# Performance work log

Hardware: AMD Instinct MI355X
Metric: run time of the kernel (lower is better)

The kernel has to match this reference:

```python
import jax, jax.numpy as jnp
import numpy as np

N_NODES = 100000
N_GRAPHS = 512


def gcn_conv(x, W, b, src, dst, n):
    # PyG GCNConv: h = x @ W; add self-loops; sym-normalize; scatter-add to dst; + bias
    h = x @ W
    loop = jnp.arange(n, dtype=src.dtype)
    s = jnp.concatenate([src, loop])
    d = jnp.concatenate([dst, loop])
    deg = jax.ops.segment_sum(jnp.ones_like(d, dtype=h.dtype), d, num_segments=n)
    dinv = jnp.where(deg > 0, jax.lax.rsqrt(deg), 0.0)
    norm = dinv[s] * dinv[d]               # [E+N]
    msg = h[s] * norm[:, None]             # gather + scale
    out = jax.ops.segment_sum(msg, d, num_segments=n)
    return out + b


def setup_inputs() -> dict:
    key = jax.random.key(0)
    ks = jax.random.split(key, 12)
    F_in, H, C = 128, 128, 10
    x = jax.random.normal(ks[0], (N_NODES, F_in), dtype=jnp.float32)
    edge_index = jax.random.randint(ks[1], (2, 3200000), 0, N_NODES, dtype=jnp.int64)
    batch = jnp.sort(jax.random.randint(ks[2], (N_NODES,), 0, N_GRAPHS, dtype=jnp.int64))
    def glorot(k, fi, fo):
        s = jnp.sqrt(6.0 / (fi + fo))
        return jax.random.uniform(k, (fi, fo), dtype=jnp.float32, minval=-s, maxval=s)
    return {
        "x": x, "edge_index": edge_index, "batch": batch,
        "W_in": glorot(ks[3], F_in, H), "b_in": jnp.zeros((H,), jnp.float32),
        "W_h0": glorot(ks[4], H, H), "b_h0": jnp.zeros((H,), jnp.float32),
        "W_h1": glorot(ks[5], H, H), "b_h1": jnp.zeros((H,), jnp.float32),
        "W_out": glorot(ks[6], H, C), "b_out": jnp.zeros((C,), jnp.float32),
    }


def reference(x, edge_index, batch, W_in, b_in, W_h0, b_h0, W_h1, b_h1, W_out, b_out):
    src, dst = edge_index[0], edge_index[1]
    n = x.shape[0]
    h = jax.nn.relu(gcn_conv(x, W_in, b_in, src, dst, n))
    h = jax.nn.relu(gcn_conv(h, W_h0, b_h0, src, dst, n))
    h = jax.nn.relu(gcn_conv(h, W_h1, b_h1, src, dst, n))
    h = gcn_conv(h, W_out, b_out, src, dst, n)
    # global_mean_pool over graph ids
    sums = jax.ops.segment_sum(h, batch, num_segments=N_GRAPHS)
    cnts = jax.ops.segment_sum(jnp.ones((n,), h.dtype), batch, num_segments=N_GRAPHS)
    pooled = sums / jnp.maximum(cnts, 1.0)[:, None]
    return jax.nn.log_softmax(pooled, axis=-1)
```

## Files before the change

kernel.cpp:

```cpp
#include <hip/hip_runtime.h>
#include <math.h>

#define TPB 256
#define MAXDEG 80
#define SHIFT 8
#define BNODES 256
#define CAP 10240
#define EPB 4096
#define LSTR 136
#define NCHUNK 13

typedef short bf16x8 __attribute__((ext_vector_type(8)));
typedef float f32x4 __attribute__((ext_vector_type(4)));

__device__ inline unsigned short f2bf(float f) {
    unsigned u = __float_as_uint(f);
    return (unsigned short)((u + 0x7fffu + ((u >> 16) & 1u)) >> 16);
}
__device__ inline float bflo(unsigned u) { return __uint_as_float(u << 16); }
__device__ inline float bfhi(unsigned u) { return __uint_as_float(u & 0xffff0000u); }


__global__ __launch_bounds__(TPB) void p1_k(const int* __restrict__ src,
                                            const int* __restrict__ dst,
                                            int* __restrict__ gbcnt,
                                            int* __restrict__ buckets, int E, int nb) {
    __shared__ int hist[512];
    __shared__ int lcur[512];
    int tid = threadIdx.x;
    for (int b = tid; b < nb; b += TPB) hist[b] = 0;
    __syncthreads();
    int e0 = blockIdx.x * EPB;
    int m = E - e0; if (m > EPB) m = EPB;
    for (int i = tid; i < m; i += TPB)
        atomicAdd(&hist[dst[e0 + i] >> SHIFT], 1);
    __syncthreads();
    for (int b = tid; b < nb; b += TPB) {
        int h = hist[b];
        lcur[b] = h ? atomicAdd(&gbcnt[b], h) : 0;
    }
    __syncthreads();
    for (int i = tid; i < m; i += TPB) {
        int d = dst[e0 + i];
        int s = src[e0 + i];
        int b = d >> SHIFT;
        int pos = atomicAdd(&lcur[b], 1);
        if (pos < CAP) buckets[(size_t)b * CAP + pos] = (s << SHIFT) | (d & (BNODES - 1));
    }
}


__global__ __launch_bounds__(TPB) void p2_k(const int* __restrict__ gbcnt,
                                            const int* __restrict__ buckets,
                                            int* __restrict__ csr,
                                            int* __restrict__ deg,
                                            float* __restrict__ dinv, int n) {
    __shared__ int cnt[BNODES][NCHUNK];
    int b = blockIdx.x, tid = threadIdx.x;
    for (int i = tid; i < BNODES * NCHUNK; i += TPB) ((int*)cnt)[i] = 0;
    __syncthreads();
    int m = gbcnt[b]; if (m > CAP) m = CAP;
    const int* bp = buckets + (size_t)b * CAP;
    int vb = b << SHIFT;
    for (int i = tid; i < m; i += TPB) {
        int rec = bp[i];
        atomicAdd(&cnt[rec & (BNODES - 1)][(rec >> SHIFT) >> 13], 1);
    }
    __syncthreads();
    {
        int run = 0;
#pragma unroll
        for (int c = 0; c < NCHUNK; c++) { int t = cnt[tid][c]; cnt[tid][c] = run; run += t; }
        int v = vb + tid;
        if (v < n) {
            deg[v] = run < MAXDEG ? run : MAXDEG;
            dinv[v] = rsqrtf((float)(run + 1));
        }
    }
    __syncthreads();
    for (int i = tid; i < m; i += TPB) {
        int rec = bp[i];
        int dl = rec & (BNODES - 1);
        int s = rec >> SHIFT;
        int pos = atomicAdd(&cnt[dl][s >> 13], 1);
        if (pos < MAXDEG) csr[(size_t)(vb + dl) * MAXDEG + pos] = s;
    }
}


__global__ __launch_bounds__(TPB) void wcast_k(const float* __restrict__ W0,
                                               const float* __restrict__ W1,
                                               const float* __restrict__ W2,
                                               const float* __restrict__ W3,
                                               unsigned short* __restrict__ T0,
                                               unsigned short* __restrict__ T1,
                                               unsigned short* __restrict__ T2,
                                               unsigned short* __restrict__ T3) {
    int b = blockIdx.x;
    if (b < 3) {
        const float* W = b == 0 ? W0 : (b == 1 ? W1 : W2);
        unsigned short* T = b == 0 ? T0 : (b == 1 ? T1 : T2);
        for (int idx = threadIdx.x; idx < 16384; idx += TPB) {
            int nn = idx >> 7, kk = idx & 127;
            T[idx] = f2bf(W[kk * 128 + nn]);
        }
    } else {
        for (int idx = threadIdx.x; idx < 2048; idx += TPB) {
            int nn = idx >> 7, kk = idx & 127;
            T3[idx] = nn < 10 ? f2bf(W3[kk * 10 + nn]) : (unsigned short)0;
        }
    }
}


__device__ __forceinline__ void mfma_tile(const unsigned short* Hs,
                                          const unsigned short* __restrict__ WT,
                                          const float* __restrict__ dinv,
                                          unsigned short* __restrict__ gout,
                                          int vb, int n, int w, int l) {
    f32x4 acc[2][8];
#pragma unroll
    for (int a = 0; a < 2; a++)
#pragma unroll
        for (int b = 0; b < 8; b++)
#pragma unroll
            for (int j = 0; j < 4; j++) acc[a][b][j] = 0.f;
    const int quad = l >> 4, lm = l & 15;
    const int mrow0 = w * 32;
#pragma unroll
    for (int ks = 0; ks < 4; ks++) {
        bf16x8 a0 = *(const bf16x8*)(Hs + (mrow0 + lm) * LSTR + ks * 32 + quad * 8);
        bf16x8 a1 = *(const bf16x8*)(Hs + (mrow0 + 16 + lm) * LSTR + ks * 32 + quad * 8);
#pragma unroll
        for (int nt = 0; nt < 8; nt++) {
            bf16x8 bf = *(const bf16x8*)(WT + (size_t)(nt * 16 + lm) * 128 + ks * 32 + quad * 8);
            acc[0][nt] = __builtin_amdgcn_mfma_f32_16x16x32_bf16(a0, bf, acc[0][nt], 0, 0, 0);
            acc[1][nt] = __builtin_amdgcn_mfma_f32_16x16x32_bf16(a1, bf, acc[1][nt], 0, 0, 0);
        }
    }
#pragma unroll
    for (int mt = 0; mt < 2; mt++) {
#pragma unroll
        for (int j = 0; j < 4; j++) {
            int r = vb + mrow0 + mt * 16 + quad * 4 + j;
            if (r < n) {
                float s = dinv[r];
#pragma unroll
                for (int nt = 0; nt < 8; nt++)
                    gout[(size_t)r * 128 + nt * 16 + lm] = f2bf(acc[mt][nt][j] * s);
            }
        }
    }
}


__global__ __launch_bounds__(256) void gemm_f32in(const float* __restrict__ x,
                                                  const unsigned short* __restrict__ WT,
                                                  const float* __restrict__ dinv,
                                                  unsigned short* __restrict__ gout, int n) {
    __shared__ unsigned short Hs[128 * LSTR];
    int tid = threadIdx.x;
    int vb = blockIdx.x * 128;
    for (int i = tid; i < 8192; i += 256) {
        int row = i >> 6, cw = i & 63;
        int gr = vb + row; if (gr > n - 1) gr = n - 1;
        float2 xv = *(const float2*)(x + (size_t)gr * 128 + cw * 2);
        unsigned pk = ((unsigned)f2bf(xv.y) << 16) | f2bf(xv.x);
        *(unsigned*)(Hs + row * LSTR + cw * 2) = pk;
    }
    __syncthreads();
    mfma_tile(Hs, WT, dinv, gout, vb, n, tid >> 6, tid & 63);
}


__global__ __launch_bounds__(256) void gemm_bf16in(const unsigned* __restrict__ hin,
                                                   const unsigned short* __restrict__ WT,
                                                   const float* __restrict__ dinv,
                                                   unsigned short* __restrict__ gout, int n) {
    __shared__ unsigned short Hs[128 * LSTR];
    int tid = threadIdx.x;
    int vb = blockIdx.x * 128;
    for (int i = tid; i < 8192; i += 256) {
        int row = i >> 6, cw = i & 63;
        int gr = vb + row; if (gr > n - 1) gr = n - 1;
        *(unsigned*)(Hs + row * LSTR + cw * 2) = hin[(size_t)gr * 64 + cw];
    }
    __syncthreads();
    mfma_tile(Hs, WT, dinv, gout, vb, n, tid >> 6, tid & 63);
}


__global__ __launch_bounds__(256) void thin_mfma(const unsigned* __restrict__ hin,
                                                 const unsigned short* __restrict__ WT3,
                                                 const float* __restrict__ dinv,
                                                 float* __restrict__ g4, int n) {
    __shared__ unsigned short Hs[128 * LSTR];
    int tid = threadIdx.x;
    int vb = blockIdx.x * 128;
    for (int i = tid; i < 8192; i += 256) {
        int row = i >> 6, cw = i & 63;
        int gr = vb + row; if (gr > n - 1) gr = n - 1;
        *(unsigned*)(Hs + row * LSTR + cw * 2) = hin[(size_t)gr * 64 + cw];
    }
    __syncthreads();
    int w = tid >> 6, l = tid & 63;
    int quad = l >> 4, lm = l & 15;
    int mrow0 = w * 32;
    f32x4 acc[2];
#pragma unroll
    for (int a = 0; a < 2; a++)
#pragma unroll
        for (int j = 0; j < 4; j++) acc[a][j] = 0.f;
#pragma unroll
    for (int ks = 0; ks < 4; ks++) {
        bf16x8 a0 = *(const bf16x8*)(Hs + (mrow0 + lm) * LSTR + ks * 32 + quad * 8);
        bf16x8 a1 = *(const bf16x8*)(Hs + (mrow0 + 16 + lm) * LSTR + ks * 32 + quad * 8);
        bf16x8 bf = *(const bf16x8*)(WT3 + (size_t)lm * 128 + ks * 32 + quad * 8);
        acc[0] = __builtin_amdgcn_mfma_f32_16x16x32_bf16(a0, bf, acc[0], 0, 0, 0);
        acc[1] = __builtin_amdgcn_mfma_f32_16x16x32_bf16(a1, bf, acc[1], 0, 0, 0);
    }
    if (lm < 10) {
#pragma unroll
        for (int mt = 0; mt < 2; mt++)
#pragma unroll
            for (int j = 0; j < 4; j++) {
                int r = vb + mrow0 + mt * 16 + quad * 4 + j;
                if (r < n) g4[(size_t)r * 10 + lm] = dinv[r] * acc[mt][j];
            }
    }
}


__global__ __launch_bounds__(256) void aggb_k(const unsigned* __restrict__ g,
                                              const float* __restrict__ dinv,
                                              const int* __restrict__ deg,
                                              const int* __restrict__ csr,
                                              const float* __restrict__ bias,
                                              unsigned* __restrict__ hout, int n) {
    int w = __builtin_amdgcn_readfirstlane((int)(threadIdx.x >> 6));
    int l = threadIdx.x & 63;
    int v = blockIdx.x * 4 + w;
    if (v >= n) return;
    unsigned u = g[(size_t)v * 64 + l];
    float acc0 = bflo(u), acc1 = bfhi(u);
    const int* cp = csr + (size_t)v * MAXDEG;
    int d = deg[v];
    int e = 0;
    for (; e + 8 <= d; e += 8) {
        int s0 = cp[e], s1 = cp[e + 1], s2 = cp[e + 2], s3 = cp[e + 3];
        int s4 = cp[e + 4], s5 = cp[e + 5], s6 = cp[e + 6], s7 = cp[e + 7];
        unsigned u0 = g[(size_t)s0 * 64 + l];
        unsigned u1 = g[(size_t)s1 * 64 + l];
        unsigned u2 = g[(size_t)s2 * 64 + l];
        unsigned u3 = g[(size_t)s3 * 64 + l];
        unsigned u4 = g[(size_t)s4 * 64 + l];
        unsigned u5 = g[(size_t)s5 * 64 + l];
        unsigned u6 = g[(size_t)s6 * 64 + l];
        unsigned u7 = g[(size_t)s7 * 64 + l];
        acc0 += (bflo(u0) + bflo(u1)) + (bflo(u2) + bflo(u3))
              + (bflo(u4) + bflo(u5)) + (bflo(u6) + bflo(u7));
        acc1 += (bfhi(u0) + bfhi(u1)) + (bfhi(u2) + bfhi(u3))
              + (bfhi(u4) + bfhi(u5)) + (bfhi(u6) + bfhi(u7));
    }
    for (; e < d; e++) {
        unsigned ux = g[(size_t)cp[e] * 64 + l];
        acc0 += bflo(ux); acc1 += bfhi(ux);
    }
    float2 bb = *(const float2*)(bias + 2 * l);
    float s = dinv[v];
    float o0 = fmaxf(s * acc0 + bb.x, 0.f);
    float o1 = fmaxf(s * acc1 + bb.y, 0.f);
    hout[(size_t)v * 64 + l] = ((unsigned)f2bf(o1) << 16) | f2bf(o0);
}


__global__ __launch_bounds__(TPB) void agg_thin(const float* __restrict__ g,
                                                const float* __restrict__ dinv,
                                                const int* __restrict__ deg,
                                                const int* __restrict__ csr,
                                                const float* __restrict__ bias,
                                                float* __restrict__ out, int n) {
    int idx = blockIdx.x * TPB + threadIdx.x;
    if (idx >= n * 10) return;
    int v = idx / 10, c = idx - v * 10;
    float acc = g[(size_t)v * 10 + c];
    size_t s0 = (size_t)v * MAXDEG;
    int d = deg[v];
    for (int e = 0; e < d; e++) acc += g[(size_t)csr[s0 + e] * 10 + c];
    out[idx] = dinv[v] * acc + bias[c];
}


#define POOL_SPAN 8

__global__ __launch_bounds__(TPB) void pool_k(const float* __restrict__ h,
                                              const int* __restrict__ batch,
                                              float* __restrict__ pool, int* __restrict__ cnt, int n) {
    __shared__ float lp[POOL_SPAN][10];
    __shared__ int lc[POOL_SPAN];
    __shared__ int g0;
    int tid = threadIdx.x;
    int v = blockIdx.x * TPB + tid;
    if (tid == 0) {
        int first = blockIdx.x * TPB;
        if (first > n - 1) first = n - 1;
        g0 = batch[first];
    }
    if (tid < POOL_SPAN) lc[tid] = 0;
    if (tid < POOL_SPAN * 10) lp[tid / 10][tid % 10] = 0.f;
    __syncthreads();
    if (v < n) {
        int gi = batch[v];
        int o = gi - g0;
        if (o < POOL_SPAN) {
            atomicAdd(&lc[o], 1);
#pragma unroll
            for (int c = 0; c < 10; c++) atomicAdd(&lp[o][c], h[(size_t)v * 10 + c]);
        } else {
            atomicAdd(&cnt[gi], 1);
#pragma unroll
            for (int c = 0; c < 10; c++) atomicAdd(&pool[gi * 10 + c], h[(size_t)v * 10 + c]);
        }
    }
    __syncthreads();
    if (tid < POOL_SPAN) {
        if (lc[tid] > 0) atomicAdd(&cnt[g0 + tid], lc[tid]);
    }
    if (tid < POOL_SPAN * 10) {
        int o = tid / 10, c = tid % 10;
        if (lc[o] > 0) atomicAdd(&pool[(g0 + o) * 10 + c], lp[o][c]);
    }
}

__global__ __launch_bounds__(TPB) void final_k(const float* __restrict__ pool,
                                               const int* __restrict__ cnt,
                                               float* __restrict__ out, int ng) {
    int gi = blockIdx.x * TPB + threadIdx.x;
    if (gi >= ng) return;
    float cn = fmaxf((float)cnt[gi], 1.f);
    float x[10];
    float m = -1e30f;
#pragma unroll
    for (int c = 0; c < 10; c++) {
        x[c] = pool[gi * 10 + c] / cn;
        m = fmaxf(m, x[c]);
    }
    float s = 0.f;
#pragma unroll
    for (int c = 0; c < 10; c++) s += expf(x[c] - m);
    float l = logf(s);
#pragma unroll
    for (int c = 0; c < 10; c++) out[gi * 10 + c] = x[c] - m - l;
}


extern "C" void kernel_launch(void* const* d_in, const int* in_sizes, int n_in,
                              void* d_out, int out_size, void* d_ws, size_t ws_size,
                              hipStream_t stream) {
    const float* x    = (const float*)d_in[0];
    const int*   ei   = (const int*)d_in[1];
    const int*   batch= (const int*)d_in[2];
    const float* W_in = (const float*)d_in[3];
    const float* b_in = (const float*)d_in[4];
    const float* W_h0 = (const float*)d_in[5];
    const float* b_h0 = (const float*)d_in[6];
    const float* W_h1 = (const float*)d_in[7];
    const float* b_h1 = (const float*)d_in[8];
    const float* W_out= (const float*)d_in[9];
    const float* b_out= (const float*)d_in[10];

    const int n  = in_sizes[2];
    const int E  = in_sizes[1] / 2;
    const int ng = out_size / 10;
    const int nb = (n + BNODES - 1) >> SHIFT;

    char* p = (char*)d_ws;
    auto carve = [&](size_t bytes) { void* r = (void*)p; p += (bytes + 255) & ~(size_t)255; return r; };
    int*            deg    = (int*)           carve((size_t)n * 4);
    float*          dinv   = (float*)         carve((size_t)n * 4);
    int*            gbcnt  = (int*)           carve((size_t)nb * 4);
    int*            buckets= (int*)           carve((size_t)nb * CAP * 4);
    int*            csr    = (int*)           carve((size_t)n * MAXDEG * 4);
    unsigned*       G      = (unsigned*)      carve((size_t)n * 64 * 4);
    unsigned*       H      = (unsigned*)      carve((size_t)n * 64 * 4);
    unsigned short* WT0    = (unsigned short*)carve(16384 * 2);
    unsigned short* WT1    = (unsigned short*)carve(16384 * 2);
    unsigned short* WT2    = (unsigned short*)carve(16384 * 2);
    unsigned short* WT3    = (unsigned short*)carve(2048 * 2);
    float*          g10    = (float*)         carve((size_t)n * 10 * 4);
    float*          h10    = (float*)         carve((size_t)n * 10 * 4);
    float*          pool   = (float*)         carve((size_t)ng * 10 * 4);
    int*            cnt    = (int*)           carve((size_t)ng * 4);

    (void)hipMemsetAsync(gbcnt, 0, (size_t)nb * 4, stream);
    (void)hipMemsetAsync(pool, 0, (size_t)ng * 10 * 4, stream);
    (void)hipMemsetAsync(cnt, 0, (size_t)ng * 4, stream);

    const int gN = (n + TPB - 1) / TPB;
    const int gP1 = (E + EPB - 1) / EPB;
    const int gG = (n + 127) / 128;
    const int gA4 = (n + 3) / 4;

    p1_k<<<gP1, TPB, 0, stream>>>(ei, ei + E, gbcnt, buckets, E, nb);
    p2_k<<<nb, TPB, 0, stream>>>(gbcnt, buckets, csr, deg, dinv, n);
    wcast_k<<<4, TPB, 0, stream>>>(W_in, W_h0, W_h1, W_out, WT0, WT1, WT2, WT3);

    gemm_f32in<<<gG, 256, 0, stream>>>(x, WT0, dinv, (unsigned short*)G, n);
    aggb_k<<<gA4, 256, 0, stream>>>(G, dinv, deg, csr, b_in, H, n);
    gemm_bf16in<<<gG, 256, 0, stream>>>(H, WT1, dinv, (unsigned short*)G, n);
    aggb_k<<<gA4, 256, 0, stream>>>(G, dinv, deg, csr, b_h0, H, n);
    gemm_bf16in<<<gG, 256, 0, stream>>>(H, WT2, dinv, (unsigned short*)G, n);
    aggb_k<<<gA4, 256, 0, stream>>>(G, dinv, deg, csr, b_h1, H, n);
    thin_mfma<<<gG, 256, 0, stream>>>(H, WT3, dinv, g10, n);
    agg_thin<<<(n * 10 + TPB - 1) / TPB, TPB, 0, stream>>>(g10, dinv, deg, csr, b_out, h10, n);
    pool_k<<<gN, TPB, 0, stream>>>(h10, batch, pool, cnt, n);
    final_k<<<(ng + TPB - 1) / TPB, TPB, 0, stream>>>(pool, cnt, (float*)d_out, ng);
}
```

Baseline: 707.0 us.

## Fold weight cast and pool zeroing into p2, pack thin layer as bf16, unroll aggregation

Weight transposition/casting and zeroing of the pool and count buffers now run as extra blocks of the CSR build kernel. This removes one kernel launch and two memsets. The final 10-wide layer output is stored as packed bf16 pairs, halving the gather traffic in the thin aggregation. The hidden-layer aggregation loop is unrolled to 16 outstanding gathers with a 4-wide tail. Together these add more memory-level parallelism at the cost of extra bf16 rounding in the last layer and more register pressure.

```diff
diff --git a/kernel.cpp b/kernel.cpp
--- a/kernel.cpp
+++ b/kernel.cpp
@@ -54,23 +54,52 @@
                                             const int* __restrict__ buckets,
                                             int* __restrict__ csr,
                                             int* __restrict__ deg,
-                                            float* __restrict__ dinv, int n) {
-    __shared__ int cnt[BNODES][NCHUNK];
+                                            float* __restrict__ dinv, int n, int nb,
+                                            const float* __restrict__ W0,
+                                            const float* __restrict__ W1,
+                                            const float* __restrict__ W2,
+                                            const float* __restrict__ W3,
+                                            unsigned short* __restrict__ T0,
+                                            unsigned short* __restrict__ T1,
+                                            unsigned short* __restrict__ T2,
+                                            unsigned short* __restrict__ T3,
+                                            float* __restrict__ pool,
+                                            int* __restrict__ cnt, int ng) {
     int b = blockIdx.x, tid = threadIdx.x;
-    for (int i = tid; i < BNODES * NCHUNK; i += TPB) ((int*)cnt)[i] = 0;
+    if (b >= nb) {
+        int widx = b - nb;
+        if (widx < 3) {
+            const float* W = widx == 0 ? W0 : (widx == 1 ? W1 : W2);
+            unsigned short* T = widx == 0 ? T0 : (widx == 1 ? T1 : T2);
+            for (int idx = tid; idx < 16384; idx += TPB) {
+                int nn = idx >> 7, kk = idx & 127;
+                T[idx] = f2bf(W[kk * 128 + nn]);
+            }
+        } else {
+            for (int idx = tid; idx < 2048; idx += TPB) {
+                int nn = idx >> 7, kk = idx & 127;
+                T3[idx] = nn < 10 ? f2bf(W3[kk * 10 + nn]) : (unsigned short)0;
+            }
+            for (int i = tid; i < ng * 10; i += TPB) pool[i] = 0.f;
+            for (int i = tid; i < ng; i += TPB) cnt[i] = 0;
+        }
+        return;
+    }
+    __shared__ int lc[BNODES][NCHUNK];
+    for (int i = tid; i < BNODES * NCHUNK; i += TPB) ((int*)lc)[i] = 0;
     __syncthreads();
     int m = gbcnt[b]; if (m > CAP) m = CAP;
     const int* bp = buckets + (size_t)b * CAP;
     int vb = b << SHIFT;
     for (int i = tid; i < m; i += TPB) {
         int rec = bp[i];
-        atomicAdd(&cnt[rec & (BNODES - 1)][(rec >> SHIFT) >> 13], 1);
+        atomicAdd(&lc[rec & (BNODES - 1)][(rec >> SHIFT) >> 13], 1);
     }
     __syncthreads();
     {
         int run = 0;
 #pragma unroll
-        for (int c = 0; c < NCHUNK; c++) { int t = cnt[tid][c]; cnt[tid][c] = run; run += t; }
+        for (int c = 0; c < NCHUNK; c++) { int t = lc[tid][c]; lc[tid][c] = run; run += t; }
         int v = vb + tid;
         if (v < n) {
             deg[v] = run < MAXDEG ? run : MAXDEG;
@@ -82,33 +111,8 @@
         int rec = bp[i];
         int dl = rec & (BNODES - 1);
         int s = rec >> SHIFT;
-        int pos = atomicAdd(&cnt[dl][s >> 13], 1);
+        int pos = atomicAdd(&lc[dl][s >> 13], 1);
         if (pos < MAXDEG) csr[(size_t)(vb + dl) * MAXDEG + pos] = s;
-    }
-}
-
-
-__global__ __launch_bounds__(TPB) void wcast_k(const float* __restrict__ W0,
-                                               const float* __restrict__ W1,
-                                               const float* __restrict__ W2,
-                                               const float* __restrict__ W3,
-                                               unsigned short* __restrict__ T0,
-                                               unsigned short* __restrict__ T1,
-                                               unsigned short* __restrict__ T2,
-                                               unsigned short* __restrict__ T3) {
-    int b = blockIdx.x;
-    if (b < 3) {
-        const float* W = b == 0 ? W0 : (b == 1 ? W1 : W2);
-        unsigned short* T = b == 0 ? T0 : (b == 1 ? T1 : T2);
-        for (int idx = threadIdx.x; idx < 16384; idx += TPB) {
-            int nn = idx >> 7, kk = idx & 127;
-            T[idx] = f2bf(W[kk * 128 + nn]);
-        }
-    } else {
-        for (int idx = threadIdx.x; idx < 2048; idx += TPB) {
-            int nn = idx >> 7, kk = idx & 127;
-            T3[idx] = nn < 10 ? f2bf(W3[kk * 10 + nn]) : (unsigned short)0;
-        }
     }
 }
 
@@ -193,7 +197,7 @@
 __global__ __launch_bounds__(256) void thin_mfma(const unsigned* __restrict__ hin,
                                                  const unsigned short* __restrict__ WT3,
                                                  const float* __restrict__ dinv,
-                                                 float* __restrict__ g4, int n) {
+                                                 unsigned* __restrict__ g4u, int n) {
     __shared__ unsigned short Hs[128 * LSTR];
     int tid = threadIdx.x;
     int vb = blockIdx.x * 128;
@@ -219,14 +223,19 @@
         acc[0] = __builtin_amdgcn_mfma_f32_16x16x32_bf16(a0, bf, acc[0], 0, 0, 0);
         acc[1] = __builtin_amdgcn_mfma_f32_16x16x32_bf16(a1, bf, acc[1], 0, 0, 0);
     }
-    if (lm < 10) {
-#pragma unroll
-        for (int mt = 0; mt < 2; mt++)
-#pragma unroll
-            for (int j = 0; j < 4; j++) {
-                int r = vb + mrow0 + mt * 16 + quad * 4 + j;
-                if (r < n) g4[(size_t)r * 10 + lm] = dinv[r] * acc[mt][j];
+#pragma unroll
+    for (int mt = 0; mt < 2; mt++) {
+#pragma unroll
+        for (int j = 0; j < 4; j++) {
+            float self = acc[mt][j];
+            float part = __shfl_down(self, 1, 64);
+            int r = vb + mrow0 + mt * 16 + quad * 4 + j;
+            if ((lm & 1) == 0 && lm < 10 && r < n) {
+                float s = dinv[r];
+                g4u[(size_t)r * 5 + (lm >> 1)] =
+                    ((unsigned)f2bf(part * s) << 16) | f2bf(self * s);
             }
+        }
     }
 }
 
@@ -246,21 +255,19 @@
     const int* cp = csr + (size_t)v * MAXDEG;
     int d = deg[v];
     int e = 0;
-    for (; e + 8 <= d; e += 8) {
-        int s0 = cp[e], s1 = cp[e + 1], s2 = cp[e + 2], s3 = cp[e + 3];
-        int s4 = cp[e + 4], s5 = cp[e + 5], s6 = cp[e + 6], s7 = cp[e + 7];
-        unsigned u0 = g[(size_t)s0 * 64 + l];
-        unsigned u1 = g[(size_t)s1 * 64 + l];
-        unsigned u2 = g[(size_t)s2 * 64 + l];
-        unsigned u3 = g[(size_t)s3 * 64 + l];
-        unsigned u4 = g[(size_t)s4 * 64 + l];
-        unsigned u5 = g[(size_t)s5 * 64 + l];
-        unsigned u6 = g[(size_t)s6 * 64 + l];
-        unsigned u7 = g[(size_t)s7 * 64 + l];
-        acc0 += (bflo(u0) + bflo(u1)) + (bflo(u2) + bflo(u3))
-              + (bflo(u4) + bflo(u5)) + (bflo(u6) + bflo(u7));
-        acc1 += (bfhi(u0) + bfhi(u1)) + (bfhi(u2) + bfhi(u3))
-              + (bfhi(u4) + bfhi(u5)) + (bfhi(u6) + bfhi(u7));
+    for (; e + 16 <= d; e += 16) {
+        unsigned uu[16];
+#pragma unroll
+        for (int j = 0; j < 16; j++) uu[j] = g[(size_t)cp[e + j] * 64 + l];
+#pragma unroll
+        for (int j = 0; j < 16; j++) { acc0 += bflo(uu[j]); acc1 += bfhi(uu[j]); }
+    }
+    for (; e + 4 <= d; e += 4) {
+        unsigned uu[4];
+#pragma unroll
+        for (int j = 0; j < 4; j++) uu[j] = g[(size_t)cp[e + j] * 64 + l];
+#pragma unroll
+        for (int j = 0; j < 4; j++) { acc0 += bflo(uu[j]); acc1 += bfhi(uu[j]); }
     }
     for (; e < d; e++) {
         unsigned ux = g[(size_t)cp[e] * 64 + l];
@@ -274,20 +281,35 @@
 }
 
 
-__global__ __launch_bounds__(TPB) void agg_thin(const float* __restrict__ g,
-                                                const float* __restrict__ dinv,
-                                                const int* __restrict__ deg,
-                                                const int* __restrict__ csr,
-                                                const float* __restrict__ bias,
-                                                float* __restrict__ out, int n) {
+__global__ __launch_bounds__(TPB) void agg_thin_bf(const unsigned* __restrict__ g4u,
+                                                   const float* __restrict__ dinv,
+                                                   const int* __restrict__ deg,
+                                                   const int* __restrict__ csr,
+                                                   const float* __restrict__ bias,
+                                                   float* __restrict__ out, int n) {
     int idx = blockIdx.x * TPB + threadIdx.x;
-    if (idx >= n * 10) return;
-    int v = idx / 10, c = idx - v * 10;
-    float acc = g[(size_t)v * 10 + c];
-    size_t s0 = (size_t)v * MAXDEG;
+    if (idx >= n * 5) return;
+    int v = idx / 5, t = idx - v * 5;
+    unsigned u = g4u[(size_t)v * 5 + t];
+    float acc0 = bflo(u), acc1 = bfhi(u);
+    const int* cp = csr + (size_t)v * MAXDEG;
     int d = deg[v];
-    for (int e = 0; e < d; e++) acc += g[(size_t)csr[s0 + e] * 10 + c];
-    out[idx] = dinv[v] * acc + bias[c];
+    int e = 0;
+    for (; e + 4 <= d; e += 4) {
+        unsigned u0 = g4u[(size_t)cp[e] * 5 + t];
+        unsigned u1 = g4u[(size_t)cp[e + 1] * 5 + t];
+        unsigned u2 = g4u[(size_t)cp[e + 2] * 5 + t];
+        unsigned u3 = g4u[(size_t)cp[e + 3] * 5 + t];
+        acc0 += (bflo(u0) + bflo(u1)) + (bflo(u2) + bflo(u3));
+        acc1 += (bfhi(u0) + bfhi(u1)) + (bfhi(u2) + bfhi(u3));
+    }
+    for (; e < d; e++) {
+        unsigned ux = g4u[(size_t)cp[e] * 5 + t];
+        acc0 += bflo(ux); acc1 += bfhi(ux);
+    }
+    float s = dinv[v];
+    out[(size_t)v * 10 + 2 * t]     = s * acc0 + bias[2 * t];
+    out[(size_t)v * 10 + 2 * t + 1] = s * acc1 + bias[2 * t + 1];
 }
 
 
@@ -387,14 +409,12 @@
     unsigned short* WT1    = (unsigned short*)carve(16384 * 2);
     unsigned short* WT2    = (unsigned short*)carve(16384 * 2);
     unsigned short* WT3    = (unsigned short*)carve(2048 * 2);
-    float*          g10    = (float*)         carve((size_t)n * 10 * 4);
+    unsigned*       g4u    = (unsigned*)      carve((size_t)n * 5 * 4);
     float*          h10    = (float*)         carve((size_t)n * 10 * 4);
     float*          pool   = (float*)         carve((size_t)ng * 10 * 4);
     int*            cnt    = (int*)           carve((size_t)ng * 4);
 
     (void)hipMemsetAsync(gbcnt, 0, (size_t)nb * 4, stream);
-    (void)hipMemsetAsync(pool, 0, (size_t)ng * 10 * 4, stream);
-    (void)hipMemsetAsync(cnt, 0, (size_t)ng * 4, stream);
 
     const int gN = (n + TPB - 1) / TPB;
     const int gP1 = (E + EPB - 1) / EPB;
@@ -402,8 +422,9 @@
     const int gA4 = (n + 3) / 4;
 
     p1_k<<<gP1, TPB, 0, stream>>>(ei, ei + E, gbcnt, buckets, E, nb);
-    p2_k<<<nb, TPB, 0, stream>>>(gbcnt, buckets, csr, deg, dinv, n);
-    wcast_k<<<4, TPB, 0, stream>>>(W_in, W_h0, W_h1, W_out, WT0, WT1, WT2, WT3);
+    p2_k<<<nb + 4, TPB, 0, stream>>>(gbcnt, buckets, csr, deg, dinv, n, nb,
+                                     W_in, W_h0, W_h1, W_out, WT0, WT1, WT2, WT3,
+                                     pool, cnt, ng);
 
     gemm_f32in<<<gG, 256, 0, stream>>>(x, WT0, dinv, (unsigned short*)G, n);
     aggb_k<<<gA4, 256, 0, stream>>>(G, dinv, deg, csr, b_in, H, n);
@@ -411,8 +432,8 @@
     aggb_k<<<gA4, 256, 0, stream>>>(G, dinv, deg, csr, b_h0, H, n);
     gemm_bf16in<<<gG, 256, 0, stream>>>(H, WT2, dinv, (unsigned short*)G, n);
     aggb_k<<<gA4, 256, 0, stream>>>(G, dinv, deg, csr, b_h1, H, n);
-    thin_mfma<<<gG, 256, 0, stream>>>(H, WT3, dinv, g10, n);
-    agg_thin<<<(n * 10 + TPB - 1) / TPB, TPB, 0, stream>>>(g10, dinv, deg, csr, b_out, h10, n);
+    thin_mfma<<<gG, 256, 0, stream>>>(H, WT3, dinv, g4u, n);
+    agg_thin_bf<<<(n * 5 + TPB - 1) / TPB, TPB, 0, stream>>>(g4u, dinv, deg, csr, b_out, h10, n);
     pool_k<<<gN, TPB, 0, stream>>>(h10, batch, pool, cnt, n);
     final_k<<<(ng + TPB - 1) / TPB, TPB, 0, stream>>>(pool, cnt, (float*)d_out, ng);
 }
```

Result: faster. 663.2 us (-6.2%).
